# Kernel optimization log

Hardware: AMD Instinct MI355X
Metric: run time of the kernel (lower is better)

Reference implementation:

```python
import jax, jax.numpy as jnp
import numpy as np

CONT_F, CATE_F = 13, 26
F = CONT_F + CATE_F            # 39 total fields
D = 40                         # orig_embedding_dim
COMB = F * (F - 1) // 2        # 741 pairs
VOCAB = 100000
B = 2048
SUB0, SUB1 = 40, 5             # subnet layer sizes
H = 100                        # hidden dims
ROWS, COLS = np.triu_indices(F, k=1)  # pair index lists (i<j)


def _ln(x, w, b, eps=1e-5):
    m = jnp.mean(x, axis=-1, keepdims=True)
    v = jnp.mean((x - m) ** 2, axis=-1, keepdims=True)
    return (x - m) * jax.lax.rsqrt(v + eps) * w + b


def setup_inputs() -> dict:
    key = jax.random.key(0)
    ks = jax.random.split(key, 12)
    s = 0.05
    first_in = COMB * SUB1 + F * D  # 3705 + 1560 = 5265
    return {
        "conts": jax.random.uniform(ks[0], (B, CONT_F), jnp.float32),
        "cates": jax.random.randint(ks[1], (B, CATE_F), 0, VOCAB),
        "combs": 0,
        "emb": jax.random.normal(ks[2], (VOCAB, D), jnp.float32) * 0.01,
        "sub_w0": jax.random.normal(ks[3], (COMB, 3 * D, SUB0), jnp.float32) * s,
        "sub_b0": jax.random.normal(ks[4], (COMB, 1, SUB0), jnp.float32) * s,
        "sln0_w": jnp.ones((SUB0,), jnp.float32),
        "sln0_b": jnp.zeros((SUB0,), jnp.float32),
        "sub_w1": jax.random.normal(ks[5], (COMB, SUB0, SUB1), jnp.float32) * s,
        "sub_b1": jax.random.normal(ks[6], (COMB, 1, SUB1), jnp.float32) * s,
        "sln1_w": jnp.ones((SUB1,), jnp.float32),
        "sln1_b": jnp.zeros((SUB1,), jnp.float32),
        "fc0_w": jax.random.normal(ks[7], (first_in, H), jnp.float32) * 0.02,
        "fc0_b": jnp.zeros((H,), jnp.float32),
        "ln0_w": jnp.ones((H,), jnp.float32),
        "ln0_b": jnp.zeros((H,), jnp.float32),
        "fc1_w": jax.random.normal(ks[8], (H, H), jnp.float32) * 0.1,
        "fc1_b": jnp.zeros((H,), jnp.float32),
        "ln1_w": jnp.ones((H,), jnp.float32),
        "ln1_b": jnp.zeros((H,), jnp.float32),
        "out_w": jax.random.normal(ks[9], (H, 1), jnp.float32) * 0.1,
        "out_b": jnp.zeros((1,), jnp.float32),
    }


def reference(conts, cates, combs, emb, sub_w0, sub_b0, sln0_w, sln0_b,
              sub_w1, sub_b1, sln1_w, sln1_b, fc0_w, fc0_b, ln0_w, ln0_b,
              fc1_w, fc1_b, ln1_w, ln1_b, out_w, out_b):
    bsz = conts.shape[0]
    # continuous fields: rows 0..CONT_F-1 of the shared embedding table scaled by value
    cont_e = emb[:CONT_F][None, :, :] * conts[:, :, None]   # [B, 13, 40]
    cate_e = emb[cates]                                      # [B, 26, 40]
    e = jnp.concatenate([cont_e, cate_e], axis=1)            # [B, 39, 40]
    # gather feature pairs
    p = e[:, ROWS]                                           # [B, 741, 40]
    q = e[:, COLS]                                           # [B, 741, 40]
    z = jnp.concatenate([p, q, p * q], axis=2)               # [B, 741, 120]
    z = jnp.transpose(z, (1, 0, 2))                          # [741, B, 120]
    # per-pair micro-MLP with shared LayerNorm params + ReLU
    z = jax.nn.relu(_ln(jnp.einsum('cbi,cio->cbo', z, sub_w0) + sub_b0, sln0_w, sln0_b))
    z = jax.nn.relu(_ln(jnp.einsum('cbi,cio->cbo', z, sub_w1) + sub_b1, sln1_w, sln1_b))
    z = jnp.transpose(z, (1, 0, 2)).reshape(bsz, -1)         # [B, 3705]
    X = jnp.concatenate([e.reshape(bsz, -1), z], axis=1)     # [B, 5265]
    X = jax.nn.relu(_ln(X @ fc0_w + fc0_b, ln0_w, ln0_b))
    X = jax.nn.relu(_ln(X @ fc1_w + fc1_b, ln1_w, ln1_b))
    return jax.nn.sigmoid(X @ out_w + out_b)                 # [B, 1]
```

## Files before the change

### kernel.cpp

```cpp
#include <hip/hip_runtime.h>

#define CONT_F 13
#define CATE_F 26
#define FF 39
#define DD 40
#define NCOMB 741
#define BB 2048
#define SUB0 40
#define SUB1 5
#define HH 100
#define K0 1560
#define KTOT 5265
#define XSTRIDE 5280
#define NPART 15
#define KCH 351
#define CPX 93

__global__ __launch_bounds__(256) void build_e_kernel(
    const float* __restrict__ conts, const int* __restrict__ cates,
    const float* __restrict__ emb, float* __restrict__ X)
{
    const int idx = blockIdx.x * 256 + threadIdx.x;
    const int d4 = idx % 10;
    const int f  = (idx / 10) % FF;
    const int b  = idx / (10 * FF);
    float4 val;
    if (f < CONT_F) {
        const float4 em = ((const float4*)(emb + f * DD))[d4];
        const float cv  = conts[b * CONT_F + f];
        val = make_float4(em.x * cv, em.y * cv, em.z * cv, em.w * cv);
    } else {
        const int tok = cates[b * CATE_F + (f - CONT_F)];
        val = ((const float4*)(emb + (size_t)tok * DD))[d4];
    }
    ((float4*)(X + (size_t)b * XSTRIDE))[f * 10 + d4] = val;
}

__global__ __launch_bounds__(256) void subnet_kernel(
    const float* __restrict__ X_in, const float* __restrict__ w0,
    const float* __restrict__ b0, const float* __restrict__ sln0w,
    const float* __restrict__ sln0b, const float* __restrict__ w1,
    const float* __restrict__ b1, const float* __restrict__ sln1w,
    const float* __restrict__ sln1b, float* __restrict__ X_out)
{
    const int wgid   = blockIdx.x;
    const int xcd    = wgid & 7;
    const int within = wgid >> 3;
    const int c_loc  = within % CPX;
    const int tl     = within / CPX;
    const int c      = xcd * CPX + c_loc;
    if (c >= NCOMB) return;
    const int row = tl * 256 + threadIdx.x;

    int r = 0, rem = c;
    while (rem >= FF - 1 - r) { rem -= FF - 1 - r; ++r; }
    const int s = r + 1 + rem;

    const float4* pr = (const float4*)(X_in + (size_t)row * XSTRIDE + r * DD);
    const float4* qr = (const float4*)(X_in + (size_t)row * XSTRIDE + s * DD);
    const float*  wc = w0 + c * (3 * DD * SUB0);
    const float*  bc = b0 + c * SUB0;

    float acc[SUB0];
    #pragma unroll
    for (int o = 0; o < SUB0; ++o) acc[o] = bc[o];

    for (int d4 = 0; d4 < DD / 4; ++d4) {
        const float4 pv4 = pr[d4];
        const float4 qv4 = qr[d4];
        #define DO_D(comp, dd) { \
            const float pv = pv4.comp, qv = qv4.comp, pq = pv * qv; \
            const float* wA = wc + (d4 * 4 + dd) * SUB0; \
            _Pragma("unroll") \
            for (int o = 0; o < SUB0; ++o) { \
                float a = acc[o]; \
                a = fmaf(wA[o],        pv, a); \
                a = fmaf(wA[1600 + o], qv, a); \
                a = fmaf(wA[3200 + o], pq, a); \
                acc[o] = a; } }
        DO_D(x, 0) DO_D(y, 1) DO_D(z, 2) DO_D(w, 3)
        #undef DO_D
    }

    float m = 0.f;
    #pragma unroll
    for (int o = 0; o < SUB0; ++o) m += acc[o];
    m *= (1.f / SUB0);
    float v = 0.f;
    #pragma unroll
    for (int o = 0; o < SUB0; ++o) { const float dl = acc[o] - m; v += dl * dl; }
    v *= (1.f / SUB0);
    const float inv = rsqrtf(v + 1e-5f);
    float h[SUB0];
    #pragma unroll
    for (int o = 0; o < SUB0; ++o) {
        const float t = (acc[o] - m) * inv * sln0w[o] + sln0b[o];
        h[o] = t > 0.f ? t : 0.f;
    }

    const float* w1c = w1 + c * (SUB0 * SUB1);
    float a2[SUB1];
    #pragma unroll
    for (int j = 0; j < SUB1; ++j) a2[j] = b1[c * SUB1 + j];
    #pragma unroll
    for (int k = 0; k < SUB0; ++k) {
        #pragma unroll
        for (int j = 0; j < SUB1; ++j)
            a2[j] = fmaf(w1c[k * SUB1 + j], h[k], a2[j]);
    }

    float m2 = 0.f;
    #pragma unroll
    for (int j = 0; j < SUB1; ++j) m2 += a2[j];
    m2 *= (1.f / SUB1);
    float v2 = 0.f;
    #pragma unroll
    for (int j = 0; j < SUB1; ++j) { const float dl = a2[j] - m2; v2 += dl * dl; }
    v2 *= (1.f / SUB1);
    const float inv2 = rsqrtf(v2 + 1e-5f);

    float* zo = X_out + (size_t)row * XSTRIDE + K0 + c * SUB1;
    #pragma unroll
    for (int j = 0; j < SUB1; ++j) {
        const float t = (a2[j] - m2) * inv2 * sln1w[j] + sln1b[j];
        zo[j] = t > 0.f ? t : 0.f;
    }
}

__global__ __launch_bounds__(256) void fc0_partial_kernel(
    const float* __restrict__ X, const float* __restrict__ w,
    float* __restrict__ partial)
{
    const int rt   = blockIdx.x;
    const int kc   = blockIdx.y;
    const int rloc = threadIdx.x & 63;
    const int ogrp = threadIdx.x >> 6;
    const int row  = rt * 64 + rloc;
    const int ob   = ogrp * 25;

    const float* xr = X + (size_t)row * XSTRIDE + kc * KCH;
    const float* wr = w + (size_t)(kc * KCH) * HH + ob;

    float acc[25];
    #pragma unroll
    for (int j = 0; j < 25; ++j) acc[j] = 0.f;

    for (int i = 0; i < KCH; ++i) {
        const float xv = xr[i];
        const float* wk = wr + (size_t)i * HH;
        #pragma unroll
        for (int j = 0; j < 25; ++j) acc[j] = fmaf(wk[j], xv, acc[j]);
    }
    float* po = partial + ((size_t)kc * BB + row) * HH + ob;
    #pragma unroll
    for (int j = 0; j < 25; ++j) po[j] = acc[j];
}

__global__ __launch_bounds__(256) void fc0rh_kernel(
    const float* __restrict__ partial, const float* __restrict__ fc0b,
    const float* __restrict__ ln0w, const float* __restrict__ ln0b,
    const float* __restrict__ fc1w, const float* __restrict__ fc1b,
    const float* __restrict__ ln1w, const float* __restrict__ ln1b,
    const float* __restrict__ outw, const float* __restrict__ outb,
    float* __restrict__ out)
{
    __shared__ float xs[4][104];
    const int wl   = threadIdx.x >> 6;
    const int lane = threadIdx.x & 63;
    const int row  = blockIdx.x * 4 + wl;

    float s0 = fc0b[lane];
    float s1 = (lane < 36) ? fc0b[64 + lane] : 0.f;
    #pragma unroll
    for (int p = 0; p < NPART; ++p) {
        const float* pr = partial + ((size_t)p * BB + row) * HH;
        s0 += pr[lane];
        if (lane < 36) s1 += pr[64 + lane];
    }
    float sum = s0 + ((lane < 36) ? s1 : 0.f);
    #pragma unroll
    for (int off = 32; off; off >>= 1) sum += __shfl_xor(sum, off, 64);
    float m  = sum * 0.01f;
    float d0 = s0 - m;
    float d1 = (lane < 36) ? (s1 - m) : 0.f;
    float vs = d0 * d0 + d1 * d1;
    #pragma unroll
    for (int off = 32; off; off >>= 1) vs += __shfl_xor(vs, off, 64);
    float inv = rsqrtf(vs * 0.01f + 1e-5f);
    {
        float x0 = d0 * inv * ln0w[lane] + ln0b[lane];
        xs[wl][lane] = x0 > 0.f ? x0 : 0.f;
        if (lane < 36) {
            float x1 = d1 * inv * ln0w[64 + lane] + ln0b[64 + lane];
            xs[wl][64 + lane] = x1 > 0.f ? x1 : 0.f;
        }
    }

    float a0 = fc1b[lane];
    float a1 = (lane < 36) ? fc1b[64 + lane] : 0.f;
    for (int k = 0; k < HH; ++k) {
        const float xv = xs[wl][k];
        a0 = fmaf(fc1w[k * HH + lane], xv, a0);
        if (lane < 36) a1 = fmaf(fc1w[k * HH + 64 + lane], xv, a1);
    }
    sum = a0 + ((lane < 36) ? a1 : 0.f);
    #pragma unroll
    for (int off = 32; off; off >>= 1) sum += __shfl_xor(sum, off, 64);
    m  = sum * 0.01f;
    d0 = a0 - m;
    d1 = (lane < 36) ? (a1 - m) : 0.f;
    vs = d0 * d0 + d1 * d1;
    #pragma unroll
    for (int off = 32; off; off >>= 1) vs += __shfl_xor(vs, off, 64);
    inv = rsqrtf(vs * 0.01f + 1e-5f);

    float x0 = d0 * inv * ln1w[lane] + ln1b[lane];
    x0 = x0 > 0.f ? x0 : 0.f;
    float t = x0 * outw[lane];
    if (lane < 36) {
        float x1 = d1 * inv * ln1w[64 + lane] + ln1b[64 + lane];
        x1 = x1 > 0.f ? x1 : 0.f;
        t = fmaf(x1, outw[64 + lane], t);
    }
    #pragma unroll
    for (int off = 32; off; off >>= 1) t += __shfl_xor(t, off, 64);
    if (lane == 0) {
        const float z = t + outb[0];
        out[row] = 1.f / (1.f + expf(-z));
    }
}

extern "C" void kernel_launch(void* const* d_in, const int* in_sizes, int n_in,
                              void* d_out, int out_size, void* d_ws, size_t ws_size,
                              hipStream_t stream)
{
    const float* conts = (const float*)d_in[0];
    const int*   cates = (const int*)d_in[1];
    const float* emb   = (const float*)d_in[3];
    const float* w0    = (const float*)d_in[4];
    const float* b0    = (const float*)d_in[5];
    const float* sln0w = (const float*)d_in[6];
    const float* sln0b = (const float*)d_in[7];
    const float* w1    = (const float*)d_in[8];
    const float* b1    = (const float*)d_in[9];
    const float* sln1w = (const float*)d_in[10];
    const float* sln1b = (const float*)d_in[11];
    const float* fc0w  = (const float*)d_in[12];
    const float* fc0b  = (const float*)d_in[13];
    const float* ln0w  = (const float*)d_in[14];
    const float* ln0b  = (const float*)d_in[15];
    const float* fc1w  = (const float*)d_in[16];
    const float* fc1b  = (const float*)d_in[17];
    const float* ln1w  = (const float*)d_in[18];
    const float* ln1b  = (const float*)d_in[19];
    const float* outw  = (const float*)d_in[20];
    const float* outb  = (const float*)d_in[21];
    float* out = (float*)d_out;

    float* X       = (float*)d_ws;
    float* partial = X + (size_t)BB * XSTRIDE;

    build_e_kernel<<<(BB * FF * 10) / 256, 256, 0, stream>>>(conts, cates, emb, X);
    subnet_kernel<<<CPX * 8 * 8, 256, 0, stream>>>(
        X, w0, b0, sln0w, sln0b, w1, b1, sln1w, sln1b, X);
    fc0_partial_kernel<<<dim3(BB / 64, NPART), 256, 0, stream>>>(X, fc0w, partial);
    fc0rh_kernel<<<BB / 4, 256, 0, stream>>>(
        partial, fc0b, ln0w, ln0b, fc1w, fc1b, ln1w, ln1b, outw, outb, out);
}
```

Measured before the change: 487.8 us.

## Transpose activation buffer to feature-major layout and process two rows per subnet thread

The intermediate activation matrix is stored transposed (feature-major, batch contiguous), so the embedding builder, the per-pair subnet and the fc0 partial GEMM all read and write coalesced along the batch dimension instead of strided rows. Each subnet thread now handles two adjacent batch columns, reusing every weight load across both and halving the block size. The fc0 partial kernel stages its outputs through shared memory to write them coalesced. The cost is higher register pressure from doubled accumulators in the subnet, plus strided scattered stores in the embedding builder.

After: 392.5 us. 19.5% less time.

```diff
diff --git a/kernel.cpp b/kernel.cpp
--- a/kernel.cpp
+++ b/kernel.cpp
@@ -11,37 +11,44 @@
 #define HH 100
 #define K0 1560
 #define KTOT 5265
-#define XSTRIDE 5280
 #define NPART 15
 #define KCH 351
 #define CPX 93
 
-__global__ __launch_bounds__(256) void build_e_kernel(
+
+__global__ __launch_bounds__(256) void build_eT_kernel(
     const float* __restrict__ conts, const int* __restrict__ cates,
-    const float* __restrict__ emb, float* __restrict__ X)
-{
-    const int idx = blockIdx.x * 256 + threadIdx.x;
-    const int d4 = idx % 10;
-    const int f  = (idx / 10) % FF;
-    const int b  = idx / (10 * FF);
-    float4 val;
+    const float* __restrict__ emb, float* __restrict__ XT)
+{
+    const int f = blockIdx.x;
+    const int b = blockIdx.y * 256 + threadIdx.x;
+    float* xo = XT + (size_t)(f * DD) * BB + b;
     if (f < CONT_F) {
-        const float4 em = ((const float4*)(emb + f * DD))[d4];
-        const float cv  = conts[b * CONT_F + f];
-        val = make_float4(em.x * cv, em.y * cv, em.z * cv, em.w * cv);
+        const float cv = conts[b * CONT_F + f];
+        const float* em = emb + f * DD;
+        #pragma unroll
+        for (int d = 0; d < DD; ++d)
+            xo[(size_t)d * BB] = em[d] * cv;
     } else {
         const int tok = cates[b * CATE_F + (f - CONT_F)];
-        val = ((const float4*)(emb + (size_t)tok * DD))[d4];
-    }
-    ((float4*)(X + (size_t)b * XSTRIDE))[f * 10 + d4] = val;
-}
-
-__global__ __launch_bounds__(256) void subnet_kernel(
-    const float* __restrict__ X_in, const float* __restrict__ w0,
+        const float4* er = (const float4*)(emb + (size_t)tok * DD);
+        #pragma unroll
+        for (int d4 = 0; d4 < DD / 4; ++d4) {
+            const float4 v = er[d4];
+            xo[(size_t)(d4 * 4 + 0) * BB] = v.x;
+            xo[(size_t)(d4 * 4 + 1) * BB] = v.y;
+            xo[(size_t)(d4 * 4 + 2) * BB] = v.z;
+            xo[(size_t)(d4 * 4 + 3) * BB] = v.w;
+        }
+    }
+}
+
+__global__ __launch_bounds__(128) void subnetT_kernel(
+    const float* __restrict__ XT, const float* __restrict__ w0,
     const float* __restrict__ b0, const float* __restrict__ sln0w,
     const float* __restrict__ sln0b, const float* __restrict__ w1,
     const float* __restrict__ b1, const float* __restrict__ sln1w,
-    const float* __restrict__ sln1b, float* __restrict__ X_out)
+    const float* __restrict__ sln1b, float* __restrict__ XTz)
 {
     const int wgid   = blockIdx.x;
     const int xcd    = wgid & 7;
@@ -50,110 +57,125 @@
     const int tl     = within / CPX;
     const int c      = xcd * CPX + c_loc;
     if (c >= NCOMB) return;
-    const int row = tl * 256 + threadIdx.x;
+    const int col = tl * 256 + threadIdx.x * 2;
 
     int r = 0, rem = c;
     while (rem >= FF - 1 - r) { rem -= FF - 1 - r; ++r; }
     const int s = r + 1 + rem;
 
-    const float4* pr = (const float4*)(X_in + (size_t)row * XSTRIDE + r * DD);
-    const float4* qr = (const float4*)(X_in + (size_t)row * XSTRIDE + s * DD);
-    const float*  wc = w0 + c * (3 * DD * SUB0);
-    const float*  bc = b0 + c * SUB0;
-
-    float acc[SUB0];
-    #pragma unroll
-    for (int o = 0; o < SUB0; ++o) acc[o] = bc[o];
-
-    for (int d4 = 0; d4 < DD / 4; ++d4) {
-        const float4 pv4 = pr[d4];
-        const float4 qv4 = qr[d4];
-        #define DO_D(comp, dd) { \
-            const float pv = pv4.comp, qv = qv4.comp, pq = pv * qv; \
-            const float* wA = wc + (d4 * 4 + dd) * SUB0; \
-            _Pragma("unroll") \
-            for (int o = 0; o < SUB0; ++o) { \
-                float a = acc[o]; \
-                a = fmaf(wA[o],        pv, a); \
-                a = fmaf(wA[1600 + o], qv, a); \
-                a = fmaf(wA[3200 + o], pq, a); \
-                acc[o] = a; } }
-        DO_D(x, 0) DO_D(y, 1) DO_D(z, 2) DO_D(w, 3)
-        #undef DO_D
-    }
-
-    float m = 0.f;
-    #pragma unroll
-    for (int o = 0; o < SUB0; ++o) m += acc[o];
-    m *= (1.f / SUB0);
-    float v = 0.f;
-    #pragma unroll
-    for (int o = 0; o < SUB0; ++o) { const float dl = acc[o] - m; v += dl * dl; }
-    v *= (1.f / SUB0);
-    const float inv = rsqrtf(v + 1e-5f);
-    float h[SUB0];
-    #pragma unroll
-    for (int o = 0; o < SUB0; ++o) {
-        const float t = (acc[o] - m) * inv * sln0w[o] + sln0b[o];
-        h[o] = t > 0.f ? t : 0.f;
-    }
+    const float* Pr = XT + (size_t)(r * DD) * BB + col;
+    const float* Qr = XT + (size_t)(s * DD) * BB + col;
+    const float* wc = w0 + c * (3 * DD * SUB0);
+    const float* bc = b0 + c * SUB0;
+
+    float acc0[SUB0], acc1[SUB0];
+    #pragma unroll
+    for (int o = 0; o < SUB0; ++o) { acc0[o] = bc[o]; acc1[o] = bc[o]; }
+
+    #pragma unroll 4
+    for (int d = 0; d < DD; ++d) {
+        const float2 pv = *(const float2*)(Pr + (size_t)d * BB);
+        const float2 qv = *(const float2*)(Qr + (size_t)d * BB);
+        const float pq0 = pv.x * qv.x, pq1 = pv.y * qv.y;
+        const float* wA = wc + d * SUB0;
+        #pragma unroll
+        for (int o = 0; o < SUB0; ++o) {
+            const float wp = wA[o], wq = wA[1600 + o], wx = wA[3200 + o];
+            float a0 = acc0[o], a1 = acc1[o];
+            a0 = fmaf(wp, pv.x, a0);  a1 = fmaf(wp, pv.y, a1);
+            a0 = fmaf(wq, qv.x, a0);  a1 = fmaf(wq, qv.y, a1);
+            a0 = fmaf(wx, pq0, a0);   a1 = fmaf(wx, pq1, a1);
+            acc0[o] = a0; acc1[o] = a1;
+        }
+    }
+
+    #define LN40(acc) { \
+        float m = 0.f; \
+        _Pragma("unroll") for (int o = 0; o < SUB0; ++o) m += acc[o]; \
+        m *= (1.f / SUB0); \
+        float v = 0.f; \
+        _Pragma("unroll") for (int o = 0; o < SUB0; ++o) { const float dl = acc[o] - m; v += dl * dl; } \
+        v *= (1.f / SUB0); \
+        const float inv = rsqrtf(v + 1e-5f); \
+        _Pragma("unroll") for (int o = 0; o < SUB0; ++o) { \
+            const float t = (acc[o] - m) * inv * sln0w[o] + sln0b[o]; \
+            acc[o] = t > 0.f ? t : 0.f; } }
+    LN40(acc0)
+    LN40(acc1)
+    #undef LN40
 
     const float* w1c = w1 + c * (SUB0 * SUB1);
-    float a2[SUB1];
-    #pragma unroll
-    for (int j = 0; j < SUB1; ++j) a2[j] = b1[c * SUB1 + j];
+    float a20[SUB1], a21[SUB1];
+    #pragma unroll
+    for (int j = 0; j < SUB1; ++j) { a20[j] = b1[c * SUB1 + j]; a21[j] = a20[j]; }
     #pragma unroll
     for (int k = 0; k < SUB0; ++k) {
         #pragma unroll
-        for (int j = 0; j < SUB1; ++j)
-            a2[j] = fmaf(w1c[k * SUB1 + j], h[k], a2[j]);
-    }
-
-    float m2 = 0.f;
-    #pragma unroll
-    for (int j = 0; j < SUB1; ++j) m2 += a2[j];
-    m2 *= (1.f / SUB1);
-    float v2 = 0.f;
-    #pragma unroll
-    for (int j = 0; j < SUB1; ++j) { const float dl = a2[j] - m2; v2 += dl * dl; }
-    v2 *= (1.f / SUB1);
-    const float inv2 = rsqrtf(v2 + 1e-5f);
-
-    float* zo = X_out + (size_t)row * XSTRIDE + K0 + c * SUB1;
+        for (int j = 0; j < SUB1; ++j) {
+            const float wv = w1c[k * SUB1 + j];
+            a20[j] = fmaf(wv, acc0[k], a20[j]);
+            a21[j] = fmaf(wv, acc1[k], a21[j]);
+        }
+    }
+
+    #define LN5(a2) { \
+        float m2 = 0.f; \
+        _Pragma("unroll") for (int j = 0; j < SUB1; ++j) m2 += a2[j]; \
+        m2 *= (1.f / SUB1); \
+        float v2 = 0.f; \
+        _Pragma("unroll") for (int j = 0; j < SUB1; ++j) { const float dl = a2[j] - m2; v2 += dl * dl; } \
+        v2 *= (1.f / SUB1); \
+        const float inv2 = rsqrtf(v2 + 1e-5f); \
+        _Pragma("unroll") for (int j = 0; j < SUB1; ++j) \
+            a2[j] = fmaxf((a2[j] - m2) * inv2 * sln1w[j] + sln1b[j], 0.f); }
+    LN5(a20)
+    LN5(a21)
+    #undef LN5
+
+    float* zo = XTz + (size_t)(K0 + c * SUB1) * BB + col;
     #pragma unroll
     for (int j = 0; j < SUB1; ++j) {
-        const float t = (a2[j] - m2) * inv2 * sln1w[j] + sln1b[j];
-        zo[j] = t > 0.f ? t : 0.f;
-    }
-}
-
-__global__ __launch_bounds__(256) void fc0_partial_kernel(
-    const float* __restrict__ X, const float* __restrict__ w,
+        float2 st; st.x = a20[j]; st.y = a21[j];
+        *(float2*)(zo + (size_t)j * BB) = st;
+    }
+}
+
+__global__ __launch_bounds__(256) void fc0_partialT_kernel(
+    const float* __restrict__ XT, const float* __restrict__ w,
     float* __restrict__ partial)
 {
+    __shared__ float st[64][105];
     const int rt   = blockIdx.x;
     const int kc   = blockIdx.y;
     const int rloc = threadIdx.x & 63;
-    const int ogrp = threadIdx.x >> 6;
+    const int ob   = __builtin_amdgcn_readfirstlane((threadIdx.x >> 6) * 25);
     const int row  = rt * 64 + rloc;
-    const int ob   = ogrp * 25;
-
-    const float* xr = X + (size_t)row * XSTRIDE + kc * KCH;
+
+    const float* xr = XT + (size_t)(kc * KCH) * BB + row;
     const float* wr = w + (size_t)(kc * KCH) * HH + ob;
 
     float acc[25];
     #pragma unroll
     for (int j = 0; j < 25; ++j) acc[j] = 0.f;
 
+    #pragma unroll 3
     for (int i = 0; i < KCH; ++i) {
-        const float xv = xr[i];
+        const float xv = xr[(size_t)i * BB];
         const float* wk = wr + (size_t)i * HH;
         #pragma unroll
         for (int j = 0; j < 25; ++j) acc[j] = fmaf(wk[j], xv, acc[j]);
     }
-    float* po = partial + ((size_t)kc * BB + row) * HH + ob;
-    #pragma unroll
-    for (int j = 0; j < 25; ++j) po[j] = acc[j];
+    #pragma unroll
+    for (int j = 0; j < 25; ++j) st[rloc][ob + j] = acc[j];
+    __syncthreads();
+
+    float* po = partial + ((size_t)kc * BB + rt * 64) * HH;
+    #pragma unroll
+    for (int k = 0; k < 25; ++k) {
+        const int idx = k * 256 + threadIdx.x;
+        const int rr = idx / 100, hh = idx % 100;
+        po[idx] = st[rr][hh];
+    }
 }
 
 __global__ __launch_bounds__(256) void fc0rh_kernel(
@@ -257,13 +279,13 @@
     const float* outb  = (const float*)d_in[21];
     float* out = (float*)d_out;
 
-    float* X       = (float*)d_ws;
-    float* partial = X + (size_t)BB * XSTRIDE;
-
-    build_e_kernel<<<(BB * FF * 10) / 256, 256, 0, stream>>>(conts, cates, emb, X);
-    subnet_kernel<<<CPX * 8 * 8, 256, 0, stream>>>(
-        X, w0, b0, sln0w, sln0b, w1, b1, sln1w, sln1b, X);
-    fc0_partial_kernel<<<dim3(BB / 64, NPART), 256, 0, stream>>>(X, fc0w, partial);
+    float* XT      = (float*)d_ws;
+    float* partial = XT + (size_t)KTOT * BB;
+
+    build_eT_kernel<<<dim3(FF, BB / 256), 256, 0, stream>>>(conts, cates, emb, XT);
+    subnetT_kernel<<<8 * CPX * 8, 128, 0, stream>>>(
+        XT, w0, b0, sln0w, sln0b, w1, b1, sln1w, sln1b, XT);
+    fc0_partialT_kernel<<<dim3(BB / 64, NPART), 256, 0, stream>>>(XT, fc0w, partial);
     fc0rh_kernel<<<BB / 4, 256, 0, stream>>>(
         partial, fc0b, ln0w, ln0b, fc1w, fc1b, ln1w, ln1b, outw, outb, out);
 }
```
